# Optimization experiments

Hardware: AMD Instinct MI355X
Metric: run time of the kernel (lower is better)

Reference implementation:

```python
import jax, jax.numpy as jnp
import numpy as np
from jax.scipy.linalg import expm
jax.config.update("jax_enable_x64", True)

HBAR = 0.6582119569
CM2EV = 0.00012398419
N6A, N10A = 4, 4
DT = 1.0
KDC = dict(E_S1=3.995, E_S2=4.9183, om6a=596.0 * CM2EV, om10a=919.0 * CM2EV,
           kap6a_S1=-0.0964, kap6a_S2=0.1193, lam=0.1825, gamma=-0.018)


def _build():
    cd = np.complex128

    def ladder(n):
        a = np.zeros((n, n), dtype=cd)
        for k in range(1, n):
            a[k - 1, k] = np.sqrt(float(k))
        adag = a.conj().T
        return (a + adag) / np.sqrt(2.0), adag @ a, np.eye(n, dtype=cd)

    Q6a1, N6a1, I6a = ladder(N6A)
    Q10a1, N10a1, I10a = ladder(N10A)
    Nel, Dvib = 3, N6A * N10A
    Ivib = np.eye(Dvib, dtype=cd)
    Iel = np.eye(Nel, dtype=cd)
    lift = lambda op: np.kron(Iel, op)
    Q6a = lift(np.kron(Q6a1, I10a))
    Q10a = lift(np.kron(I6a, Q10a1))
    N6a = lift(np.kron(N6a1, I10a))
    N10a = lift(np.kron(I6a, N10a1))
    P = []
    for k in range(Nel):
        ek = np.zeros(Nel, dtype=cd); ek[k] = 1.0
        P.append(np.kron(np.outer(ek, ek), Ivib))
    e1 = np.zeros(Nel, dtype=cd); e1[1] = 1.0
    e2 = np.zeros(Nel, dtype=cd); e2[2] = 1.0
    Poff = np.kron(np.outer(e1, e2) + np.outer(e2, e1), Ivib)
    Lj = np.kron(np.outer(e1, e2), Ivib)  # |S1><S2| lift
    D = Nel * Dvib
    I = np.eye(D, dtype=cd)
    p = KDC
    H = (p['E_S1'] * P[1] + p['E_S2'] * P[2] + p['om6a'] * N6a + p['om10a'] * N10a
         + p['kap6a_S1'] * P[1] @ Q6a + p['kap6a_S2'] * P[2] @ Q6a
         + p['lam'] * Poff @ Q10a + p['gamma'] * Poff @ (Q10a @ Q10a))
    # Coherent part -i(I kron H - H^T* kron I); dissipator at unit rate (scaled by g later)
    Lc = -1j * (np.kron(I, H) - np.kron(H.conj().T, I))
    LdL = Lj.conj().T @ Lj
    Ld0 = (np.kron(Lj.conj(), Lj) - 0.5 * np.kron(I, LdL)
           - 0.5 * np.kron(LdL.conj().T, I))
    psi = np.zeros(D, dtype=cd); psi[2 * N6A * N10A] = 1.0
    rho0 = np.outer(psi, psi.conj()).reshape(-1)
    trP = np.stack([P[k].T.reshape(-1) for k in range(3)])  # [3, D^2]
    return Lc, Ld0, rho0, trP

_LC, _LD0, _RHO0, _TRP = _build()


def setup_inputs() -> dict:
    return {"log_g": jnp.asarray(np.log(1.0 / 40.0), dtype=jnp.float32),
            "n_steps": 1000}


def reference(log_g, n_steps):
    Lc = jnp.asarray(_LC)
    Ld0 = jnp.asarray(_LD0)
    rho0 = jnp.asarray(_RHO0)
    trP = jnp.asarray(_TRP)
    g = jnp.exp(log_g).astype(jnp.float64)
    Lsup = Lc + g * Ld0                      # [D^2, D^2] complex128
    U = expm(Lsup * (DT / HBAR))             # one-step propagator

    def step(rho, _):
        pops = jnp.real(trP @ rho)           # tr(P_k rho), k=0..2
        return U @ rho, pops

    _, ps = jax.lax.scan(step, rho0, None, length=int(n_steps))  # [n_steps, 3]
    return (ps[:, 0].astype(jnp.float32),
            ps[:, 1].astype(jnp.float32),
            ps[:, 2].astype(jnp.float32))
```

## Files before the change

### kernel.cpp

```cpp
#include <hip/hip_runtime.h>
#include <math.h>


#define DS 1024
#define MATD ((size_t)DS * DS * sizeof(double))
#define PA 66

typedef double v4d __attribute__((ext_vector_type(4)));

__device__ inline double Qel(int i, int j) {
    if (i == j + 1) return sqrt((double)i) * 0.70710678118654752440;
    if (j == i + 1) return sqrt((double)j) * 0.70710678118654752440;
    return 0.0;
}

__device__ inline void fill_H(double* Hs, int tid) {
    const double CM2EV = 0.00012398419;
    const double E_S1 = 3.995, E_S2 = 4.9183;
    const double om6a = 596.0 * CM2EV, om10a = 919.0 * CM2EV;
    const double kapA = -0.0964, kapB = 0.1193, lam = 0.1825, gam = -0.018;
    for (int h = tid; h < 1024; h += 256) {
        int r = h >> 5, c = h & 31;
        int e = r >> 4, v6 = (r >> 2) & 3, v10 = r & 3;
        int e2 = c >> 4, w6 = (c >> 2) & 3, w10 = c & 3;
        double val = 0.0;
        if (r == c) val += (e ? E_S2 : E_S1) + om6a * v6 + om10a * v10;
        if (e == e2 && v10 == w10) val += (e ? kapB : kapA) * Qel(v6, w6);
        if (e != e2 && v6 == w6) {
            double q2 = 0.0;
            #pragma unroll
            for (int m = 0; m < 4; ++m) q2 += Qel(v10, m) * Qel(m, w10);
            val += lam * Qel(v10, w10) + gam * q2;
        }
        Hs[h] = val;
    }
}

__global__ __launch_bounds__(256)
void build_G14(const float* __restrict__ logg, double* __restrict__ X,
               double* __restrict__ Y, double* __restrict__ Z)
{
    int tid = threadIdx.x;
    if (blockIdx.x >= 4096) {
        int idx = (blockIdx.x - 4096) * 256 + tid;
        if (idx < 256 * 1024) {
            int r = idx >> 10, i = idx & 1023;
            double v = 0.0;
            if (r < 2 && i % 33 == 0) {
                int a = i / 33;
                if ((a < 16) == (r == 0)) v = 1.0;
            }
            Y[idx] = v;
        } else if (idx < 256 * 1024 + 1024) {
            int i = idx - 256 * 1024;
            Z[i] = (i == 528) ? 1.0 : 0.0;
        }
        return;
    }
    __shared__ double Hs[1024];
    fill_H(Hs, tid);
    __syncthreads();
    double g = exp((double)logg[0]);
    const double sc = ((1.0 / 0.6582119569) / 8.0) / 14.0;
    int idx = blockIdx.x * 256 + tid;
    int r = idx >> 10, c = idx & 1023;
    int i = r >> 5, j = r & 31;
    int k = c >> 5, l = c & 31;
    double t = 0.0;
    if (k <= l) {
        if (i <= j) {
            if (i < 16 && j < 16) {
                int p = i + 16, q = j + 16;
                if ((p == k && q == l) || (p == l && q == k)) t += g;
            }
            if (i == k && j == l) t -= 0.5 * g * ((i >= 16) + (j >= 16));
        } else {
            if (j == l) t += Hs[i * 32 + k];
            if (k != l && j == k) t += Hs[i * 32 + l];
            if (i == k) t -= Hs[l * 32 + j];
            if (k != l && i == l) t -= Hs[k * 32 + j];
        }
    } else {
        if (i <= j) {
            double ha = 0.0;
            if (j == l) ha += Hs[i * 32 + k];
            if (j == k) ha -= Hs[i * 32 + l];
            if (i == k) ha -= Hs[l * 32 + j];
            if (i == l) ha += Hs[k * 32 + j];
            t -= ha;
        } else {
            if (i < 16 && j < 16 && (i + 16 == k) && (j + 16 == l)) t += g;
            if (i == k && j == l) t -= 0.5 * g * ((i >= 16) + (j >= 16));
        }
    }
    X[idx] = t * sc + ((r == c) ? 1.0 : 0.0);
}

__global__ __launch_bounds__(256)
void apply_T(const float* __restrict__ logg, const double* __restrict__ M,
             double* __restrict__ O, double invk)
{
    __shared__ double Hs[1024];
    const int tid = threadIdx.x;
    fill_H(Hs, tid);
    __syncthreads();
    const double g = exp((double)logg[0]);
    const double sck = ((1.0 / 0.6582119569) / 8.0) * invk;
    const int p = ((blockIdx.x & 7) << 7) | (blockIdx.x >> 3);
    const int i = p >> 5, j = p & 31;

    double a0 = 0.0, a1 = 0.0, a2 = 0.0, a3 = 0.0;
    const int e = tid;

#define ADDROW(q, wgt) { const double* r_ = M + (size_t)(q) * DS; double w_ = (wgt); \
    a0 += w_ * r_[e]; a1 += w_ * r_[e + 256];                                        \
    a2 += w_ * r_[e + 512]; a3 += w_ * r_[e + 768]; }

    if (i <= j) {
        for (int m = 0; m < 32; ++m) {
            double c = Hs[i * 32 + m];
            if (c != 0.0 && m != j) {
                if (m > j) ADDROW(m * 32 + j, -c)
                else       ADDROW(j * 32 + m,  c)
            }
        }
        for (int m = 0; m < 32; ++m) {
            double c = Hs[m * 32 + j];
            if (c != 0.0 && m != i) {
                if (i > m) ADDROW(i * 32 + m,  c)
                else       ADDROW(m * 32 + i, -c)
            }
        }
        if (i < 16 && j < 16) ADDROW((i + 16) * 32 + (j + 16), g)
        if (i >= 16 || j >= 16)
            ADDROW(p, -0.5 * g * (double)((i >= 16) + (j >= 16)))
    } else {
        for (int m = 0; m < 32; ++m) {
            double c = Hs[i * 32 + m];
            if (c != 0.0) {
                int lo = m < j ? m : j, hi = m < j ? j : m;
                ADDROW(lo * 32 + hi, c)
            }
        }
        for (int m = 0; m < 32; ++m) {
            double c = Hs[m * 32 + j];
            if (c != 0.0) {
                int lo = m < i ? m : i, hi = m < i ? i : m;
                ADDROW(lo * 32 + hi, -c)
            }
        }
        if (i < 16 && j < 16) ADDROW((i + 16) * 32 + (j + 16), g)
        ADDROW(p, -0.5 * g * (double)((i >= 16) + (j >= 16)))
    }
#undef ADDROW

    size_t base = (size_t)p * DS;
    O[base + e]       = sck * a0 + ((p == e)       ? 1.0 : 0.0);
    O[base + e + 256] = sck * a1 + ((p == e + 256) ? 1.0 : 0.0);
    O[base + e + 512] = sck * a2 + ((p == e + 512) ? 1.0 : 0.0);
    O[base + e + 768] = sck * a3 + ((p == e + 768) ? 1.0 : 0.0);
}

__global__ __launch_bounds__(1024, 1)
void dgemm(const double* __restrict__ A, const double* __restrict__ B,
           double* __restrict__ D)
{
    __shared__ double As[64 * PA];
    __shared__ double Bs[64 * PA];
    const int tid = threadIdx.x;
    const int bm = blockIdx.x << 6, bn = blockIdx.y << 6;
    const int w = tid >> 6, lane = tid & 63;
    const int lr = lane & 15, lk = lane >> 4;
    const int p = w & 3, kg = w >> 2;
    const int wr = (p >> 1) << 5, wc = (p & 1) << 5;

    v4d acc[2][2];
    #pragma unroll
    for (int si = 0; si < 2; ++si)
        #pragma unroll
        for (int sj = 0; sj < 2; ++sj) acc[si][sj] = (v4d){0., 0., 0., 0.};

    const int ra = tid >> 4;
    const int cs = (tid & 15) << 2;
    const double* gA = A + (size_t)(bm + ra) * DS + cs;
    const double* gB = B + (size_t)ra * DS + bn + cs;
    double va[4], vb[4];
    #pragma unroll
    for (int u = 0; u < 4; ++u) { va[u] = gA[u]; vb[u] = gB[u]; }

    for (int kt = 0; kt < DS; kt += 64) {
        #pragma unroll
        for (int u = 0; u < 4; ++u) {
            As[ra * PA + cs + u] = va[u];
            Bs[ra * PA + cs + u] = vb[u];
        }
        __syncthreads();
        if (kt + 64 < DS) {
            #pragma unroll
            for (int u = 0; u < 4; ++u) {
                va[u] = gA[kt + 64 + u];
                vb[u] = gB[(size_t)(kt + 64) * DS + u];
            }
        }
        #pragma unroll
        for (int s = 0; s < 4; ++s) {
            int k = (kg << 4) + (s << 2) + lk;
            double a0 = As[(wr + lr) * PA + k];
            double a1 = As[(wr + 16 + lr) * PA + k];
            double b0 = Bs[k * PA + wc + lr];
            double b1 = Bs[k * PA + wc + 16 + lr];
            acc[0][0] = __builtin_amdgcn_mfma_f64_16x16x4f64(a0, b0, acc[0][0], 0, 0, 0);
            acc[0][1] = __builtin_amdgcn_mfma_f64_16x16x4f64(a0, b1, acc[0][1], 0, 0, 0);
            acc[1][0] = __builtin_amdgcn_mfma_f64_16x16x4f64(a1, b0, acc[1][0], 0, 0, 0);
            acc[1][1] = __builtin_amdgcn_mfma_f64_16x16x4f64(a1, b1, acc[1][1], 0, 0, 0);
        }
        __syncthreads();
    }

    double* red = As;
    if (kg == 3) {
        #pragma unroll
        for (int si = 0; si < 2; ++si)
            #pragma unroll
            for (int sj = 0; sj < 2; ++sj)
                #pragma unroll
                for (int r = 0; r < 4; ++r)
                    red[(wr + si * 16 + lk + 4 * r) * 64 + wc + sj * 16 + lr]
                        = acc[si][sj][r];
    }
    __syncthreads();
    if (kg == 2) {
        #pragma unroll
        for (int si = 0; si < 2; ++si)
            #pragma unroll
            for (int sj = 0; sj < 2; ++sj)
                #pragma unroll
                for (int r = 0; r < 4; ++r)
                    red[(wr + si * 16 + lk + 4 * r) * 64 + wc + sj * 16 + lr]
                        += acc[si][sj][r];
    }
    __syncthreads();
    if (kg == 1) {
        #pragma unroll
        for (int si = 0; si < 2; ++si)
            #pragma unroll
            for (int sj = 0; sj < 2; ++sj)
                #pragma unroll
                for (int r = 0; r < 4; ++r)
                    red[(wr + si * 16 + lk + 4 * r) * 64 + wc + sj * 16 + lr]
                        += acc[si][sj][r];
    }
    __syncthreads();
    if (kg == 0) {
        #pragma unroll
        for (int si = 0; si < 2; ++si)
            #pragma unroll
            for (int sj = 0; sj < 2; ++sj) {
                int col = bn + wc + sj * 16 + lr;
                #pragma unroll
                for (int r = 0; r < 4; ++r) {
                    int row = bm + wr + si * 16 + lk + 4 * r;
                    D[(size_t)row * DS + col] = acc[si][sj][r]
                        + red[(wr + si * 16 + lk + 4 * r) * 64 + wc + sj * 16 + lr];
                }
            }
    }
}

__global__ __launch_bounds__(256)
void ypart(const double* __restrict__ P, const double* __restrict__ Y,
           double* __restrict__ scratch, int SR)
{
    __shared__ double Yld[32 * 64];
    __shared__ double red[32 * 64];
    const int tid = threadIdx.x;
    const int cc = tid & 63, kw = tid >> 6;
    const int col = (blockIdx.x << 6) + cc;
    const int kb = blockIdx.y << 6;
    const int r0 = blockIdx.z << 5;

    for (int idx = tid; idx < 32 * 64; idx += 256) {
        int r = idx >> 6, kk = idx & 63;
        Yld[idx] = Y[(size_t)(r0 + r) * DS + kb + kk];
    }
    __syncthreads();

    double acc[32];
    #pragma unroll
    for (int r = 0; r < 32; ++r) acc[r] = 0.0;

    #pragma unroll
    for (int kk = 0; kk < 16; ++kk) {
        int kl = (kw << 4) + kk;
        double pv = P[(size_t)(kb + kl) * DS + col];
        #pragma unroll
        for (int r = 0; r < 32; ++r)
            acc[r] += Yld[(r << 6) + kl] * pv;
    }

    __syncthreads();
    if (kw == 3) {
        #pragma unroll
        for (int r = 0; r < 32; ++r) red[(r << 6) + cc] = acc[r];
    }
    __syncthreads();
    if (kw == 2) {
        #pragma unroll
        for (int r = 0; r < 32; ++r) red[(r << 6) + cc] += acc[r];
    }
    __syncthreads();
    if (kw == 1) {
        #pragma unroll
        for (int r = 0; r < 32; ++r) red[(r << 6) + cc] += acc[r];
    }
    __syncthreads();
    if (kw == 0) {
        #pragma unroll
        for (int r = 0; r < 32; ++r) red[(r << 6) + cc] += acc[r];
    }
    __syncthreads();
    for (int idx = tid; idx < 32 * 64; idx += 256) {
        int r = idx >> 6, c2 = idx & 63;
        scratch[((size_t)blockIdx.y * SR + r0 + r) * DS + (blockIdx.x << 6) + c2]
            = red[idx];
    }
}

__global__ __launch_bounds__(256)
void yreduce(const double* __restrict__ scratch, double* __restrict__ Y,
             int M, int SR)
{
    int idx = blockIdx.x * 256 + threadIdx.x;
    int r = idx >> 10, c = idx & 1023;
    double s = 0.0;
    #pragma unroll
    for (int q = 0; q < 16; ++q)
        s += scratch[((size_t)q * SR + r) * DS + c];
    Y[(size_t)(M + r) * DS + c] = s;
}

__global__ __launch_bounds__(256)
void zstep(const double* __restrict__ V, const double* __restrict__ Zin,
           double* __restrict__ Zout)
{
    int row = blockIdx.x * 4 + (threadIdx.x >> 6);
    int lane = threadIdx.x & 63;
    const double2* r_ = (const double2*)(V + (size_t)row * DS);
    const double2* z_ = (const double2*)Zin;
    double s = 0.0;
    #pragma unroll
    for (int k = 0; k < 8; ++k) {
        double2 a = r_[(k << 6) + lane];
        double2 b = z_[(k << 6) + lane];
        s += a.x * b.x + a.y * b.y;
    }
    #pragma unroll
    for (int off = 32; off; off >>= 1) s += __shfl_down(s, off);
    if (lane == 0) Zout[row] = s;
}

__global__ __launch_bounds__(128)
void final_pops(const double* __restrict__ Y, const double* __restrict__ Z,
                float* __restrict__ out, int n)
{
    int t = blockIdx.x;
    int k = threadIdx.x >> 6, lane = threadIdx.x & 63;
    int a = t & 127, j = t >> 7;
    const double* y = Y + (size_t)(2 * a + k) * 1024;
    const double* z = Z + (size_t)j * 1024;
    double s = 0.0;
    for (int i = lane; i < 1024; i += 64) s += y[i] * z[i];
    #pragma unroll
    for (int off = 32; off; off >>= 1) s += __shfl_down(s, off);
    if (lane == 0) {
        out[(size_t)(k + 1) * n + t] = (float)s;
        if (k == 0) out[t] = 0.0f;
    }
}

static inline void ydouble2(const double* P, double* Y, double* scr, int M,
                            hipStream_t stream)
{
    int gz = (M + 31) / 32; if (gz < 1) gz = 1;
    int SR = gz * 32;
    ypart<<<dim3(16, 16, gz), 256, 0, stream>>>(P, Y, scr, SR);
    yreduce<<<SR * 4, 256, 0, stream>>>(scr, Y, M, SR);
}

extern "C" void kernel_launch(void* const* d_in, const int* in_sizes, int n_in,
                              void* d_out, int out_size, void* d_ws, size_t ws_size,
                              hipStream_t stream)
{
    const float* logg = (const float*)d_in[0];
    float* out = (float*)d_out;
    const int n = out_size / 3;
    (void)in_sizes; (void)n_in; (void)ws_size;

    char* ws = (char*)d_ws;
    double* b0 = (double*)(ws + 0 * MATD);
    double* b1 = (double*)(ws + 1 * MATD);
    double* b2 = (double*)(ws + 2 * MATD);
    double* scr = (double*)(ws + 3 * MATD);
    double* Y  = (double*)(ws + 5 * MATD);
    double* Z  = Y + 256 * 1024;

    dim3 g2(16, 16);

    build_G14<<<4096 + 1028, 256, 0, stream>>>(logg, b0, Y, Z);
    double* src = b0; double* dst = b1;
    for (int k = 13; k >= 1; --k) {
        apply_T<<<1024, 256, 0, stream>>>(logg, src, dst, 1.0 / (double)k);
        double* t = src; src = dst; dst = t;
    }

    dgemm<<<g2, 1024, 0, stream>>>(b1, b1, b0);
    dgemm<<<g2, 1024, 0, stream>>>(b0, b0, b2);
    dgemm<<<g2, 1024, 0, stream>>>(b2, b2, b0);
    ydouble2(b0, Y, scr, 2, stream);
    dgemm<<<g2, 1024, 0, stream>>>(b0, b0, b1);
    ydouble2(b1, Y, scr, 4, stream);
    dgemm<<<g2, 1024, 0, stream>>>(b1, b1, b2);
    ydouble2(b2, Y, scr, 8, stream);
    dgemm<<<g2, 1024, 0, stream>>>(b2, b2, b1);
    ydouble2(b1, Y, scr, 16, stream);
    dgemm<<<g2, 1024, 0, stream>>>(b1, b1, b2);
    ydouble2(b2, Y, scr, 32, stream);
    dgemm<<<g2, 1024, 0, stream>>>(b2, b2, b1);
    ydouble2(b1, Y, scr, 64, stream);
    dgemm<<<g2, 1024, 0, stream>>>(b1, b1, b2);
    ydouble2(b2, Y, scr, 128, stream);
    dgemm<<<g2, 1024, 0, stream>>>(b2, b2, b1);

    for (int j = 1; j < 8; ++j)
        zstep<<<256, 256, 0, stream>>>(b1, Z + (size_t)(j - 1) * 1024,
                                       Z + (size_t)j * 1024);

    final_pops<<<n, 128, 0, stream>>>(Y, Z, out, n);
}
```

Measured before the change: 785.3 us.

## Double-buffer dgemm LDS tiles and rebalance Y/Z split to drop a squaring

```diff
diff --git a/kernel.cpp b/kernel.cpp
--- a/kernel.cpp
+++ b/kernel.cpp
@@ -43,7 +43,7 @@
     int tid = threadIdx.x;
     if (blockIdx.x >= 4096) {
         int idx = (blockIdx.x - 4096) * 256 + tid;
-        if (idx < 256 * 1024) {
+        if (idx < 128 * 1024) {
             int r = idx >> 10, i = idx & 1023;
             double v = 0.0;
             if (r < 2 && i % 33 == 0) {
@@ -51,8 +51,8 @@
                 if ((a < 16) == (r == 0)) v = 1.0;
             }
             Y[idx] = v;
-        } else if (idx < 256 * 1024 + 1024) {
-            int i = idx - 256 * 1024;
+        } else if (idx < 128 * 1024 + 1024) {
+            int i = idx - 128 * 1024;
             Z[i] = (i == 528) ? 1.0 : 0.0;
         }
         return;
@@ -165,8 +165,8 @@
 void dgemm(const double* __restrict__ A, const double* __restrict__ B,
            double* __restrict__ D)
 {
-    __shared__ double As[64 * PA];
-    __shared__ double Bs[64 * PA];
+    __shared__ double As[2][64 * PA];
+    __shared__ double Bs[2][64 * PA];
     const int tid = threadIdx.x;
     const int bm = blockIdx.x << 6, bn = blockIdx.y << 6;
     const int w = tid >> 6, lane = tid & 63;
@@ -187,14 +187,15 @@
     double va[4], vb[4];
     #pragma unroll
     for (int u = 0; u < 4; ++u) { va[u] = gA[u]; vb[u] = gB[u]; }
+    #pragma unroll
+    for (int u = 0; u < 4; ++u) {
+        As[0][ra * PA + cs + u] = va[u];
+        Bs[0][ra * PA + cs + u] = vb[u];
+    }
+    __syncthreads();
 
     for (int kt = 0; kt < DS; kt += 64) {
-        #pragma unroll
-        for (int u = 0; u < 4; ++u) {
-            As[ra * PA + cs + u] = va[u];
-            Bs[ra * PA + cs + u] = vb[u];
-        }
-        __syncthreads();
+        const int pb = (kt >> 6) & 1;
         if (kt + 64 < DS) {
             #pragma unroll
             for (int u = 0; u < 4; ++u) {
@@ -205,19 +206,26 @@
         #pragma unroll
         for (int s = 0; s < 4; ++s) {
             int k = (kg << 4) + (s << 2) + lk;
-            double a0 = As[(wr + lr) * PA + k];
-            double a1 = As[(wr + 16 + lr) * PA + k];
-            double b0 = Bs[k * PA + wc + lr];
-            double b1 = Bs[k * PA + wc + 16 + lr];
+            double a0 = As[pb][(wr + lr) * PA + k];
+            double a1 = As[pb][(wr + 16 + lr) * PA + k];
+            double b0 = Bs[pb][k * PA + wc + lr];
+            double b1 = Bs[pb][k * PA + wc + 16 + lr];
             acc[0][0] = __builtin_amdgcn_mfma_f64_16x16x4f64(a0, b0, acc[0][0], 0, 0, 0);
             acc[0][1] = __builtin_amdgcn_mfma_f64_16x16x4f64(a0, b1, acc[0][1], 0, 0, 0);
             acc[1][0] = __builtin_amdgcn_mfma_f64_16x16x4f64(a1, b0, acc[1][0], 0, 0, 0);
             acc[1][1] = __builtin_amdgcn_mfma_f64_16x16x4f64(a1, b1, acc[1][1], 0, 0, 0);
         }
+        if (kt + 64 < DS) {
+            #pragma unroll
+            for (int u = 0; u < 4; ++u) {
+                As[pb ^ 1][ra * PA + cs + u] = va[u];
+                Bs[pb ^ 1][ra * PA + cs + u] = vb[u];
+            }
+        }
         __syncthreads();
     }
 
-    double* red = As;
+    double* red = &As[0][0];
     if (kg == 3) {
         #pragma unroll
         for (int si = 0; si < 2; ++si)
@@ -365,7 +373,7 @@
 {
     int t = blockIdx.x;
     int k = threadIdx.x >> 6, lane = threadIdx.x & 63;
-    int a = t & 127, j = t >> 7;
+    int a = t & 63, j = t >> 6;
     const double* y = Y + (size_t)(2 * a + k) * 1024;
     const double* z = Z + (size_t)j * 1024;
     double s = 0.0;
@@ -402,11 +410,11 @@
     double* b2 = (double*)(ws + 2 * MATD);
     double* scr = (double*)(ws + 3 * MATD);
     double* Y  = (double*)(ws + 5 * MATD);
-    double* Z  = Y + 256 * 1024;
+    double* Z  = Y + 128 * 1024;
 
     dim3 g2(16, 16);
 
-    build_G14<<<4096 + 1028, 256, 0, stream>>>(logg, b0, Y, Z);
+    build_G14<<<4096 + 516, 256, 0, stream>>>(logg, b0, Y, Z);
     double* src = b0; double* dst = b1;
     for (int k = 13; k >= 1; --k) {
         apply_T<<<1024, 256, 0, stream>>>(logg, src, dst, 1.0 / (double)k);
@@ -428,11 +436,9 @@
     dgemm<<<g2, 1024, 0, stream>>>(b2, b2, b1);
     ydouble2(b1, Y, scr, 64, stream);
     dgemm<<<g2, 1024, 0, stream>>>(b1, b1, b2);
-    ydouble2(b2, Y, scr, 128, stream);
-    dgemm<<<g2, 1024, 0, stream>>>(b2, b2, b1);
-
-    for (int j = 1; j < 8; ++j)
-        zstep<<<256, 256, 0, stream>>>(b1, Z + (size_t)(j - 1) * 1024,
+
+    for (int j = 1; j < 16; ++j)
+        zstep<<<256, 256, 0, stream>>>(b2, Z + (size_t)(j - 1) * 1024,
                                        Z + (size_t)j * 1024);
 
     final_pops<<<n, 128, 0, stream>>>(Y, Z, out, n);
```

After: 707.6 us. -9.9%, faster.
